# Kernel optimization log

Measured on AMD Instinct MI355X. Metric: run time of the kernel, lower is better.

## Reference

```python
import jax, jax.numpy as jnp
import numpy as np

N_TX, N_USER = 100000, 50000
F_TX, F_USER = 128, 64
HID, H, OUT = 64, 4, 32
E = 500000
SLOPE = 0.2  # PyG GATConv default negative_slope


def _gat(x_src, x_dst, src, dst, W, a_src, a_dst, bias, heads, ch, concat, n_dst):
    # PyG GATConv (shared lin for src/dst, add_self_loops=False)
    hs = (x_src @ W).reshape(-1, heads, ch)          # [Ns,H,C]
    hd = (x_dst @ W).reshape(-1, heads, ch)          # [Nd,H,C]
    als = jnp.einsum('nhc,hc->nh', hs, a_src)        # alpha_src per node
    ald = jnp.einsum('nhc,hc->nh', hd, a_dst)
    e = jax.nn.leaky_relu(als[src] + ald[dst], SLOPE)        # [E,H]
    emax = jax.ops.segment_max(e, dst, num_segments=n_dst)   # softmax per dst
    ex = jnp.exp(e - emax[dst])
    den = jax.ops.segment_sum(ex, dst, num_segments=n_dst)
    alpha = ex / (den[dst] + 1e-16)
    out = jax.ops.segment_sum(hs[src] * alpha[:, :, None], dst, num_segments=n_dst)
    out = out.reshape(n_dst, heads * ch) if concat else out.mean(axis=1)
    return out + bias


def setup_inputs() -> dict:
    key = jax.random.key(0)
    ks = iter(jax.random.split(key, 40))
    def nrm(shape, s=0.05):
        return jax.random.normal(next(ks), shape, dtype=jnp.float32) * s
    inp = {}
    inp['x_tx'] = jax.random.normal(next(ks), (N_TX, F_TX), dtype=jnp.float32)
    inp['x_user'] = jax.random.normal(next(ks), (N_USER, F_USER), dtype=jnp.float32)
    src_u = jax.random.randint(next(ks), (E,), 0, N_USER)
    dst_t = jax.random.randint(next(ks), (E,), 0, N_TX)
    inp['ei_u2t'] = jnp.stack([src_u, dst_t]).astype(jnp.int32)
    src_t = jax.random.randint(next(ks), (E,), 0, N_TX)
    dst_u = jax.random.randint(next(ks), (E,), 0, N_USER)
    inp['ei_t2u'] = jnp.stack([src_t, dst_u]).astype(jnp.int32)
    inp['Wp_tx'] = nrm((F_TX, HID)); inp['bp_tx'] = jnp.zeros((HID,), jnp.float32)
    inp['Wp_user'] = nrm((F_USER, HID)); inp['bp_user'] = jnp.zeros((HID,), jnp.float32)
    for et in ('u2t', 't2u'):
        inp[f'W1_{et}'] = nrm((HID, H * HID))
        inp[f'as1_{et}'] = nrm((H, HID)); inp[f'ad1_{et}'] = nrm((H, HID))
        inp[f'b1_{et}'] = jnp.zeros((H * HID,), jnp.float32)
        inp[f'W2_{et}'] = nrm((H * HID, OUT))
        inp[f'as2_{et}'] = nrm((1, OUT)); inp[f'ad2_{et}'] = nrm((1, OUT))
        inp[f'b2_{et}'] = jnp.zeros((OUT,), jnp.float32)
    inp['Wc'] = nrm((OUT, 1)); inp['bc'] = jnp.zeros((1,), jnp.float32)
    return inp


def reference(x_tx, x_user, ei_u2t, ei_t2u, Wp_tx, bp_tx, Wp_user, bp_user,
              W1_u2t, as1_u2t, ad1_u2t, b1_u2t, W1_t2u, as1_t2u, ad1_t2u, b1_t2u,
              W2_u2t, as2_u2t, ad2_u2t, b2_u2t, W2_t2u, as2_t2u, ad2_t2u, b2_t2u,
              Wc, bc):
    elu = jax.nn.elu
    h_tx = elu(x_tx @ Wp_tx + bp_tx)
    h_us = elu(x_user @ Wp_user + bp_user)
    # conv1: heads=H, concat=True (HeteroConv sum -> each dst has one edge type)
    t1 = _gat(h_us, h_tx, ei_u2t[0], ei_u2t[1], W1_u2t, as1_u2t, ad1_u2t, b1_u2t, H, HID, True, N_TX)
    u1 = _gat(h_tx, h_us, ei_t2u[0], ei_t2u[1], W1_t2u, as1_t2u, ad1_t2u, b1_t2u, H, HID, True, N_USER)
    t1, u1 = elu(t1), elu(u1)
    # conv2: heads=1, concat=False; only 'transaction' output feeds classifier
    t2 = elu(_gat(u1, t1, ei_u2t[0], ei_u2t[1], W2_u2t, as2_u2t, ad2_u2t, b2_u2t, 1, OUT, False, N_TX))
    return (t2 @ Wc + bc)[:, 0]
```

## Files before the change

### kernel.cpp

```cpp
#include <hip/hip_runtime.h>
#include <hip/hip_bf16.h>
#include <math.h>

#define N_TX   100000
#define N_USER 50000
#define F_TX   128
#define F_USER 64
#define HID    64
#define NH     4
#define OUTC   32
#define NE     500000
#define HC1    256
#define SLOPE  0.2f
#define NB_T   391
#define NB_U   196

__device__ __forceinline__ float elu_f(float x) { return x > 0.f ? x : (expf(x) - 1.f); }
__device__ __forceinline__ float lrelu_exp_fast(float x) { x = x > 0.f ? x : SLOPE * x; return __expf(x); }

__global__ __launch_bounds__(256) void gemm_kernel(const float* __restrict__ A,
    const float* __restrict__ B, const float* __restrict__ bias,
    float* __restrict__ C, int N, int K, int M, int act)
{
    __shared__ float As[16][65];
    __shared__ float Bs[16][65];
    const int tid = threadIdx.x;
    const int tx = tid % 16, ty = tid / 16;
    const int row0 = blockIdx.y * 64, col0 = blockIdx.x * 64;
    float acc[4][4] = {};
    for (int k0 = 0; k0 < K; k0 += 16) {
        #pragma unroll
        for (int i = 0; i < 4; ++i) {
            int idx = tid * 4 + i;
            int r = idx >> 4, kk = idx & 15;
            int gr = row0 + r;
            As[kk][r] = (gr < N) ? A[(size_t)gr * K + (k0 + kk)] : 0.f;
        }
        #pragma unroll
        for (int i = 0; i < 4; ++i) {
            int idx = tid * 4 + i;
            int kk = idx >> 6, c = idx & 63;
            int gc = col0 + c;
            Bs[kk][c] = (gc < M) ? B[(size_t)(k0 + kk) * M + gc] : 0.f;
        }
        __syncthreads();
        #pragma unroll
        for (int kk = 0; kk < 16; ++kk) {
            float a4[4], b4[4];
            #pragma unroll
            for (int i = 0; i < 4; ++i) a4[i] = As[kk][ty * 4 + i];
            #pragma unroll
            for (int j = 0; j < 4; ++j) b4[j] = Bs[kk][tx * 4 + j];
            #pragma unroll
            for (int i = 0; i < 4; ++i)
                #pragma unroll
                for (int j = 0; j < 4; ++j) acc[i][j] += a4[i] * b4[j];
        }
        __syncthreads();
    }
    #pragma unroll
    for (int i = 0; i < 4; ++i) {
        int r = row0 + ty * 4 + i;
        if (r >= N) continue;
        #pragma unroll
        for (int j = 0; j < 4; ++j) {
            int c = col0 + tx * 4 + j;
            if (c >= M) continue;
            float v = acc[i][j] + (bias ? bias[c] : 0.f);
            if (act == 1) v = elu_f(v);
            C[(size_t)r * M + c] = v;
        }
    }
}

__global__ __launch_bounds__(256) void gemm_proj_attn(const float* __restrict__ A,
    const float* __restrict__ B, const float* __restrict__ bias,
    float* __restrict__ C, int N, int K,
    const float* __restrict__ Ma, float* __restrict__ oa,
    const float* __restrict__ Mb, float* __restrict__ ob)
{
    __shared__ float As[16][65];
    __shared__ float Bs[16][65];
    const int tid = threadIdx.x;
    const int tx = tid % 16, ty = tid / 16;
    const int row0 = blockIdx.y * 64;
    float acc[4][4] = {};
    for (int k0 = 0; k0 < K; k0 += 16) {
        #pragma unroll
        for (int i = 0; i < 4; ++i) {
            int idx = tid * 4 + i;
            int r = idx >> 4, kk = idx & 15;
            int gr = row0 + r;
            As[kk][r] = (gr < N) ? A[(size_t)gr * K + (k0 + kk)] : 0.f;
        }
        #pragma unroll
        for (int i = 0; i < 4; ++i) {
            int idx = tid * 4 + i;
            int kk = idx >> 6, c = idx & 63;
            Bs[kk][c] = B[(size_t)(k0 + kk) * 64 + c];
        }
        __syncthreads();
        #pragma unroll
        for (int kk = 0; kk < 16; ++kk) {
            float a4[4], b4[4];
            #pragma unroll
            for (int i = 0; i < 4; ++i) a4[i] = As[kk][ty * 4 + i];
            #pragma unroll
            for (int j = 0; j < 4; ++j) b4[j] = Bs[kk][tx * 4 + j];
            #pragma unroll
            for (int i = 0; i < 4; ++i)
                #pragma unroll
                for (int j = 0; j < 4; ++j) acc[i][j] += a4[i] * b4[j];
        }
        __syncthreads();
    }
    const float4 ma0 = *(const float4*)(Ma + (tx * 4 + 0) * 4);
    const float4 ma1 = *(const float4*)(Ma + (tx * 4 + 1) * 4);
    const float4 ma2 = *(const float4*)(Ma + (tx * 4 + 2) * 4);
    const float4 ma3 = *(const float4*)(Ma + (tx * 4 + 3) * 4);
    const float4 mb0 = *(const float4*)(Mb + (tx * 4 + 0) * 4);
    const float4 mb1 = *(const float4*)(Mb + (tx * 4 + 1) * 4);
    const float4 mb2 = *(const float4*)(Mb + (tx * 4 + 2) * 4);
    const float4 mb3 = *(const float4*)(Mb + (tx * 4 + 3) * 4);
    const float4 bb  = *(const float4*)(bias + tx * 4);
    #pragma unroll
    for (int i = 0; i < 4; ++i) {
        int r = row0 + ty * 4 + i;
        bool wr = (r < N);
        float v0 = acc[i][0] + bb.x; v0 = v0 > 0.f ? v0 : (expf(v0) - 1.f);
        float v1 = acc[i][1] + bb.y; v1 = v1 > 0.f ? v1 : (expf(v1) - 1.f);
        float v2 = acc[i][2] + bb.z; v2 = v2 > 0.f ? v2 : (expf(v2) - 1.f);
        float v3 = acc[i][3] + bb.w; v3 = v3 > 0.f ? v3 : (expf(v3) - 1.f);
        if (wr) *(float4*)(C + (size_t)r * 64 + tx * 4) = make_float4(v0, v1, v2, v3);
        float pax = v0 * ma0.x + v1 * ma1.x + v2 * ma2.x + v3 * ma3.x;
        float pay = v0 * ma0.y + v1 * ma1.y + v2 * ma2.y + v3 * ma3.y;
        float paz = v0 * ma0.z + v1 * ma1.z + v2 * ma2.z + v3 * ma3.z;
        float paw = v0 * ma0.w + v1 * ma1.w + v2 * ma2.w + v3 * ma3.w;
        float pbx = v0 * mb0.x + v1 * mb1.x + v2 * mb2.x + v3 * mb3.x;
        float pby = v0 * mb0.y + v1 * mb1.y + v2 * mb2.y + v3 * mb3.y;
        float pbz = v0 * mb0.z + v1 * mb1.z + v2 * mb2.z + v3 * mb3.z;
        float pbw = v0 * mb0.w + v1 * mb1.w + v2 * mb2.w + v3 * mb3.w;
        #pragma unroll
        for (int off = 1; off < 16; off <<= 1) {
            pax += __shfl_xor(pax, off); pay += __shfl_xor(pay, off);
            paz += __shfl_xor(paz, off); paw += __shfl_xor(paw, off);
            pbx += __shfl_xor(pbx, off); pby += __shfl_xor(pby, off);
            pbz += __shfl_xor(pbz, off); pbw += __shfl_xor(pbw, off);
        }
        if (tx == 0 && wr) {
            *(float4*)(oa + (size_t)r * 4) = make_float4(pax, pay, paz, paw);
            *(float4*)(ob + (size_t)r * 4) = make_float4(pbx, pby, pbz, pbw);
        }
    }
}

struct AVArgs  { const float* W; const float* a; float* out; int K; int H; int C; };
struct AVArgs6 { AVArgs t[6]; };

__global__ void attn_vecs_kernel(AVArgs6 args)
{
    AVArgs A = args.t[blockIdx.x];
    int tid = threadIdx.x;
    if (tid < A.K * A.H) {
        int k = tid % A.K, h = tid / A.K;
        float s = 0.f;
        const float* wrow = A.W + (size_t)k * (A.H * A.C) + h * A.C;
        const float* arow = A.a + h * A.C;
        for (int c = 0; c < A.C; ++c) s += wrow[c] * arow[c];
        A.out[k * A.H + h] = s;
    }
}

__global__ __launch_bounds__(256) void hist2_kernel(const int* __restrict__ dst_t,
    const int* __restrict__ dst_u, int* __restrict__ deg_t, int* __restrict__ deg_u)
{
    int e = blockIdx.x * 256 + threadIdx.x;
    if (e < NE) atomicAdd(&deg_t[dst_t[e]], 1);
    else {
        e -= NE;
        if (e < NE) atomicAdd(&deg_u[dst_u[e]], 1);
    }
}

__global__ __launch_bounds__(256) void block_sum2_kernel(const int* __restrict__ deg_t,
    int* __restrict__ bsum_t, const int* __restrict__ deg_u, int* __restrict__ bsum_u)
{
    __shared__ int lds[256];
    int b = blockIdx.x, t = threadIdx.x;
    const int* deg; int* bsum; int Nd, lb;
    if (b < NB_T) { deg = deg_t; bsum = bsum_t; Nd = N_TX; lb = b; }
    else         { deg = deg_u; bsum = bsum_u; Nd = N_USER; lb = b - NB_T; }
    int i = lb * 256 + t;
    lds[t] = (i < Nd) ? deg[i] : 0;
    __syncthreads();
    for (int o = 128; o > 0; o >>= 1) {
        if (t < o) lds[t] += lds[t + o];
        __syncthreads();
    }
    if (t == 0) bsum[lb] = lds[0];
}

__global__ __launch_bounds__(512) void scan_bsum2_kernel(int* __restrict__ bt,
    int* __restrict__ bu)
{
    __shared__ int lds[512];
    int t = threadIdx.x;
    {
        int v = (t < NB_T) ? bt[t] : 0;
        lds[t] = v;
        __syncthreads();
        for (int o = 1; o < 512; o <<= 1) {
            int x = (t >= o) ? lds[t - o] : 0;
            __syncthreads();
            lds[t] += x;
            __syncthreads();
        }
        if (t < NB_T) bt[t] = lds[t] - v;
        __syncthreads();
    }
    {
        int v = (t < NB_U) ? bu[t] : 0;
        lds[t] = v;
        __syncthreads();
        for (int o = 1; o < 512; o <<= 1) {
            int x = (t >= o) ? lds[t - o] : 0;
            __syncthreads();
            lds[t] += x;
            __syncthreads();
        }
        if (t < NB_U) bu[t] = lds[t] - v;
    }
}

__global__ __launch_bounds__(256) void scan_final2_kernel(
    const int* __restrict__ deg_t, const int* __restrict__ be_t,
    int* __restrict__ rowptr_t, int* __restrict__ cur_t,
    const int* __restrict__ deg_u, const int* __restrict__ be_u,
    int* __restrict__ rowptr_u, int* __restrict__ cur_u)
{
    __shared__ int lds[256];
    int b = blockIdx.x, t = threadIdx.x;
    const int* deg; const int* be; int* rowptr; int* cursor; int Nd, lb;
    if (b < NB_T) { deg = deg_t; be = be_t; rowptr = rowptr_t; cursor = cur_t; Nd = N_TX; lb = b; }
    else         { deg = deg_u; be = be_u; rowptr = rowptr_u; cursor = cur_u; Nd = N_USER; lb = b - NB_T; }
    int i = lb * 256 + t;
    int v = (i < Nd) ? deg[i] : 0;
    lds[t] = v;
    __syncthreads();
    for (int o = 1; o < 256; o <<= 1) {
        int x = (t >= o) ? lds[t - o] : 0;
        __syncthreads();
        lds[t] += x;
        __syncthreads();
    }
    int excl = lds[t] - v + be[lb];
    if (i < Nd) {
        rowptr[i] = excl;
        cursor[i] = excl;
        if (i == Nd - 1) rowptr[Nd] = NE;
    }
}

__global__ __launch_bounds__(256) void scatter2_ew_kernel(
    const int* __restrict__ src_t, const int* __restrict__ dst_t,
    int* __restrict__ cur_t, int* __restrict__ csr_t, float* __restrict__ ew_t,
    const float* __restrict__ als_t, const float* __restrict__ ald_t,
    const int* __restrict__ src_u, const int* __restrict__ dst_u,
    int* __restrict__ cur_u, int* __restrict__ csr_u, float* __restrict__ ew_u,
    const float* __restrict__ als_u, const float* __restrict__ ald_u)
{
    int e = blockIdx.x * 256 + threadIdx.x;
    const int* srcA; const int* dstA; int* cur; int* csr; float* ew;
    const float* als; const float* ald;
    if (e < NE) {
        srcA = src_t; dstA = dst_t; cur = cur_t; csr = csr_t; ew = ew_t;
        als = als_t; ald = ald_t;
    } else {
        e -= NE;
        if (e >= NE) return;
        srcA = src_u; dstA = dst_u; cur = cur_u; csr = csr_u; ew = ew_u;
        als = als_u; ald = ald_u;
    }
    int s = srcA[e], d = dstA[e];
    int p = atomicAdd(&cur[d], 1);
    csr[p] = s;
    float4 a = *(const float4*)(als + (size_t)s * 4);
    float4 b = *(const float4*)(ald + (size_t)d * 4);
    float4 w;
    w.x = lrelu_exp_fast(a.x + b.x);
    w.y = lrelu_exp_fast(a.y + b.y);
    w.z = lrelu_exp_fast(a.z + b.z);
    w.w = lrelu_exp_fast(a.w + b.w);
    *(float4*)(ew + (size_t)p * 4) = w;
}

__device__ __forceinline__ void acc_edge(int s, int i, int lane,
    const float* __restrict__ ew, const float* __restrict__ hsrc,
    float& a0, float& a1, float& a2, float& a3,
    float& w0, float& w1, float& w2, float& w3)
{
    float4 e = *(const float4*)(ew + (size_t)i * 4);
    float x = hsrc[(size_t)s * 64 + lane];
    a0 = fmaf(e.x, x, a0); w0 += e.x;
    a1 = fmaf(e.y, x, a1); w1 += e.y;
    a2 = fmaf(e.z, x, a2); w2 += e.z;
    a3 = fmaf(e.w, x, a3); w3 += e.w;
}

__global__ __launch_bounds__(256) void agg_conv1_kernel(const int* __restrict__ rowptr,
    const int* __restrict__ csr, const float* __restrict__ hsrc,
    const float* __restrict__ ew, float* __restrict__ agg, int Nd)
{
    int d = blockIdx.x * 4 + (threadIdx.x >> 6);
    int lane = threadIdx.x & 63;
    if (d >= Nd) return;
    int beg = rowptr[d], end = rowptr[d + 1];
    float a0 = 0.f, a1 = 0.f, a2 = 0.f, a3 = 0.f;
    float w0 = 0.f, w1 = 0.f, w2 = 0.f, w3 = 0.f;
    int i = beg;
    for (; i + 2 <= end; i += 2) {
        int s0 = csr[i], s1 = csr[i + 1];
        acc_edge(s0, i,     lane, ew, hsrc, a0, a1, a2, a3, w0, w1, w2, w3);
        acc_edge(s1, i + 1, lane, ew, hsrc, a0, a1, a2, a3, w0, w1, w2, w3);
    }
    if (i < end)
        acc_edge(csr[i], i, lane, ew, hsrc, a0, a1, a2, a3, w0, w1, w2, w3);
    float* o = agg + (size_t)d * 256;
    o[lane]       = a0 / (w0 + 1e-16f);
    o[64 + lane]  = a1 / (w1 + 1e-16f);
    o[128 + lane] = a2 / (w2 + 1e-16f);
    o[192 + lane] = a3 / (w3 + 1e-16f);
}

#define ACC_STEP(i, XS, WV) \
    acc[i][0] = fmaf((XS), (WV).x, acc[i][0]); \
    acc[i][1] = fmaf((XS), (WV).y, acc[i][1]); \
    acc[i][2] = fmaf((XS), (WV).z, acc[i][2]); \
    acc[i][3] = fmaf((XS), (WV).w, acc[i][3]);
#define ACC4(i, XV) \
    ACC_STEP(i, (XV).x, w0) ACC_STEP(i, (XV).y, w1) \
    ACC_STEP(i, (XV).z, w2) ACC_STEP(i, (XV).w, w3)

__global__ __launch_bounds__(256) void transform_v6(
    const float* __restrict__ agg, const float* __restrict__ W1,
    const float* __restrict__ b1, const float* __restrict__ vvec,
    float* __restrict__ dot_part, float* __restrict__ rows_out,
    int Nd, int writeRows)
{
    constexpr int SXP = 68;
    __shared__ float sX[64 * SXP];
    __shared__ float sW[64 * 64];
    const int tid  = threadIdx.x;
    const int w    = tid >> 6;
    const int lane = tid & 63;
    const int h    = blockIdx.y;
    const int base = blockIdx.x * 64;

    #pragma unroll
    for (int it = 0; it < 4; ++it) {
        int r  = w * 16 + it * 4 + (lane >> 4);
        int c0 = (lane & 15) * 4;
        int g  = base + r;
        float4 v = make_float4(0.f, 0.f, 0.f, 0.f);
        if (g < Nd) v = *(const float4*)(agg + (size_t)g * 256 + h * 64 + c0);
        *(float4*)(sX + r * SXP + c0) = v;
    }
    #pragma unroll
    for (int it = 0; it < 4; ++it) {
        int c    = w * 16 + it * 4 + (lane >> 4);
        int col0 = (lane & 15) * 4;
        *(float4*)(sW + c * 64 + col0) =
            *(const float4*)(W1 + (size_t)c * 256 + h * 64 + col0);
    }
    __syncthreads();

    const int tx = tid & 15;
    const int ty = tid >> 4;
    float acc[4][4] = {};

    #pragma unroll 1
    for (int c0 = 0; c0 < 64; c0 += 4) {
        const float4 x0 = *(const float4*)(sX + (ty * 4 + 0) * SXP + c0);
        const float4 x1 = *(const float4*)(sX + (ty * 4 + 1) * SXP + c0);
        const float4 x2 = *(const float4*)(sX + (ty * 4 + 2) * SXP + c0);
        const float4 x3 = *(const float4*)(sX + (ty * 4 + 3) * SXP + c0);
        const float4 w0 = *(const float4*)(sW + (c0 + 0) * 64 + tx * 4);
        const float4 w1 = *(const float4*)(sW + (c0 + 1) * 64 + tx * 4);
        const float4 w2 = *(const float4*)(sW + (c0 + 2) * 64 + tx * 4);
        const float4 w3 = *(const float4*)(sW + (c0 + 3) * 64 + tx * 4);
        ACC4(0, x0)
        ACC4(1, x1)
        ACC4(2, x2)
        ACC4(3, x3)
    }

    const float4 bb = *(const float4*)(b1   + h * 64 + tx * 4);
    const float4 vv = *(const float4*)(vvec + h * 64 + tx * 4);
    float* dp = dot_part + (size_t)h * Nd;
    #pragma unroll
    for (int i = 0; i < 4; ++i) {
        int g = base + ty * 4 + i;
        if (g >= Nd) continue;
        float v0 = acc[i][0] + bb.x; v0 = v0 > 0.f ? v0 : (expf(v0) - 1.f);
        float v1 = acc[i][1] + bb.y; v1 = v1 > 0.f ? v1 : (expf(v1) - 1.f);
        float v2 = acc[i][2] + bb.z; v2 = v2 > 0.f ? v2 : (expf(v2) - 1.f);
        float v3 = acc[i][3] + bb.w; v3 = v3 > 0.f ? v3 : (expf(v3) - 1.f);
        if (writeRows)
            *(float4*)(rows_out + (size_t)g * 256 + h * 64 + tx * 4) =
                make_float4(v0, v1, v2, v3);
        float s = v0 * vv.x + v1 * vv.y + v2 * vv.z + v3 * vv.w;
        s += __shfl_xor(s, 1); s += __shfl_xor(s, 2);
        s += __shfl_xor(s, 4); s += __shfl_xor(s, 8);
        if (tx == 0) dp[g] = s;
    }
}

__global__ __launch_bounds__(256) void combine_parts(
    const float* __restrict__ ap, float* __restrict__ o1, int N1,
    const float* __restrict__ bp, float* __restrict__ o2, int N2)
{
    int i = blockIdx.x * 256 + threadIdx.x;
    if (i < N1) {
        o1[i] = ap[i] + ap[N1 + i] + ap[2 * N1 + i] + ap[3 * N1 + i];
    } else {
        int j = i - N1;
        if (j < N2)
            o2[j] = bp[j] + bp[N2 + j] + bp[2 * N2 + j] + bp[3 * N2 + j];
    }
}

__global__ __launch_bounds__(256) void conv2_fused_kernel(const int* __restrict__ rowptr,
    const int* __restrict__ csr, const float* __restrict__ hs2,
    const float* __restrict__ als2, const float* __restrict__ ald2,
    const float* __restrict__ b2, const float* __restrict__ Wc, const float* __restrict__ bc,
    float* __restrict__ out, int Nd)
{
    int d = blockIdx.x * 4 + (threadIdx.x >> 6);
    int lane = threadIdx.x & 63;
    if (d >= Nd) return;
    int beg = rowptr[d], end = rowptr[d + 1];
    float aldd = ald2[d];
    int half = lane >> 5, c = lane & 31;
    float acc = 0.f, wsum = 0.f;
    for (int i = beg + half; i < end; i += 2) {
        int s = csr[i];
        float w = lrelu_exp_fast(als2[s] + aldd);
        acc = fmaf(w, hs2[(size_t)s * 32 + c], acc);
        wsum += w;
    }
    acc  += __shfl_down(acc, 32);
    wsum += __shfl_down(wsum, 32);
    float val = 0.f;
    if (lane < 32) {
        float t2 = acc / (wsum + 1e-16f) + b2[c];
        t2 = t2 > 0.f ? t2 : (expf(t2) - 1.f);
        val = t2 * Wc[c];
    }
    #pragma unroll
    for (int o = 16; o > 0; o >>= 1) val += __shfl_down(val, o);
    if (lane == 0) out[d] = val + bc[0];
}

extern "C" void kernel_launch(void* const* d_in, const int* in_sizes, int n_in,
                              void* d_out, int out_size, void* d_ws, size_t ws_size,
                              hipStream_t stream)
{
    const float* x_tx    = (const float*)d_in[0];
    const float* x_user  = (const float*)d_in[1];
    const int*   ei_u2t  = (const int*)d_in[2];
    const int*   ei_t2u  = (const int*)d_in[3];
    const float* Wp_tx   = (const float*)d_in[4];
    const float* bp_tx   = (const float*)d_in[5];
    const float* Wp_user = (const float*)d_in[6];
    const float* bp_user = (const float*)d_in[7];
    const float* W1_u2t  = (const float*)d_in[8];
    const float* as1_u2t = (const float*)d_in[9];
    const float* ad1_u2t = (const float*)d_in[10];
    const float* b1_u2t  = (const float*)d_in[11];
    const float* W2_u2t  = (const float*)d_in[12];
    const float* as2_u2t = (const float*)d_in[13];
    const float* ad2_u2t = (const float*)d_in[14];
    const float* b2_u2t  = (const float*)d_in[15];
    const float* W1_t2u  = (const float*)d_in[16];
    const float* as1_t2u = (const float*)d_in[17];
    const float* ad1_t2u = (const float*)d_in[18];
    const float* b1_t2u  = (const float*)d_in[19];
    const float* Wc      = (const float*)d_in[24];
    const float* bc      = (const float*)d_in[25];
    float* out = (float*)d_out;
    float* ws  = (float*)d_ws;

    const int* src_u2t = ei_u2t;
    const int* dst_u2t = ei_u2t + NE;
    const int* src_t2u = ei_t2u;
    const int* dst_u   = ei_t2u + NE;

    float* h_tx   = ws;
    float* h_us   = ws + 6400000;
    float* hs2    = ws + 9600000;
    float* als2   = ws + 11200000;
    float* ald2   = ws + 11250000;
    float* als_us = ws + 11350000;
    float* ald_us = ws + 11550000;
    float* als_tx = ws + 11750000;
    float* ald_tx = ws + 12150000;
    float* agg    = ws + 12550000;
    float* avec   = ws + 38150000;
    float* ald2p = hs2;
    float* als2p = hs2 + 400000;
    float* ew_t   = ws + 38152000;
    float* ew_u   = ws + 40152000;
    int* ibase    = (int*)(ws + 42152000);
    int* deg_t    = ibase;
    int* deg_u    = ibase + 100000;
    int* rowptr_t = ibase + 150000;
    int* cur_t    = ibase + 250001;
    int* csr_t    = ibase + 350001;
    int* rowptr_u = ibase + 850001;
    int* cur_u    = ibase + 900002;
    int* csr_u    = ibase + 950002;
    int* bsum_t   = ibase + 1450002;
    int* bsum_u   = ibase + 1450514;

    float* Msrc_u2t = avec + 0;
    float* Mdst_u2t = avec + 256;
    float* Msrc_t2u = avec + 512;
    float* Mdst_t2u = avec + 768;
    float* vsrc2    = avec + 1024;
    float* vdst2    = avec + 1280;

    AVArgs6 av;
    av.t[0] = { W1_u2t, as1_u2t, Msrc_u2t, HID, NH, HID };
    av.t[1] = { W1_u2t, ad1_u2t, Mdst_u2t, HID, NH, HID };
    av.t[2] = { W1_t2u, as1_t2u, Msrc_t2u, HID, NH, HID };
    av.t[3] = { W1_t2u, ad1_t2u, Mdst_t2u, HID, NH, HID };
    av.t[4] = { W2_u2t, as2_u2t, vsrc2, HC1, 1, OUTC };
    av.t[5] = { W2_u2t, ad2_u2t, vdst2, HC1, 1, OUTC };
    attn_vecs_kernel<<<6, 256, 0, stream>>>(av);

    hipMemsetAsync(deg_t, 0, 150000 * sizeof(int), stream);

    hist2_kernel<<<(2 * NE + 255) / 256, 256, 0, stream>>>(dst_u2t, dst_u, deg_t, deg_u);
    block_sum2_kernel<<<NB_T + NB_U, 256, 0, stream>>>(deg_t, bsum_t, deg_u, bsum_u);
    scan_bsum2_kernel<<<1, 512, 0, stream>>>(bsum_t, bsum_u);
    scan_final2_kernel<<<NB_T + NB_U, 256, 0, stream>>>(
        deg_t, bsum_t, rowptr_t, cur_t, deg_u, bsum_u, rowptr_u, cur_u);

    gemm_proj_attn<<<dim3(1, (N_TX + 63) / 64), 256, 0, stream>>>(
        x_tx, Wp_tx, bp_tx, h_tx, N_TX, F_TX,
        Mdst_u2t, ald_tx, Msrc_t2u, als_tx);
    gemm_proj_attn<<<dim3(1, (N_USER + 63) / 64), 256, 0, stream>>>(
        x_user, Wp_user, bp_user, h_us, N_USER, F_USER,
        Msrc_u2t, als_us, Mdst_t2u, ald_us);

    scatter2_ew_kernel<<<(2 * NE + 255) / 256, 256, 0, stream>>>(
        src_u2t, dst_u2t, cur_t, csr_t, ew_t, als_us, ald_tx,
        src_t2u, dst_u,   cur_u, csr_u, ew_u, als_tx, ald_us);

    agg_conv1_kernel<<<(N_TX + 3) / 4, 256, 0, stream>>>(
        rowptr_t, csr_t, h_us, ew_t, agg, N_TX);
    transform_v6<<<dim3((N_TX + 63) / 64, NH), 256, 0, stream>>>(
        agg, W1_u2t, b1_u2t, vdst2, ald2p, nullptr, N_TX, 0);

    agg_conv1_kernel<<<(N_USER + 3) / 4, 256, 0, stream>>>(
        rowptr_u, csr_u, h_tx, ew_u, agg, N_USER);
    transform_v6<<<dim3((N_USER + 63) / 64, NH), 256, 0, stream>>>(
        agg, W1_t2u, b1_t2u, vsrc2, als2p, agg, N_USER, 1);
    float* u1 = agg;

    combine_parts<<<(N_TX + N_USER + 255) / 256, 256, 0, stream>>>(
        ald2p, ald2, N_TX, als2p, als2, N_USER);

    gemm_kernel<<<dim3(1, (N_USER + 63) / 64), 256, 0, stream>>>(
        u1, W2_u2t, nullptr, hs2, N_USER, HC1, OUTC, 0);
    conv2_fused_kernel<<<(N_TX + 3) / 4, 256, 0, stream>>>(
        rowptr_t, csr_t, hs2, als2, ald2, b2_u2t, Wc, bc, out, N_TX);
}
```

Before: 632.8 us.

## Keep W1 columns in registers and process all heads per block in transform

Rewrites the per-head conv1 output transform. Each thread now holds one 64-element column of W1 in registers, and each wave handles one head. A block stages 32 full 256-wide rows into LDS and reads them as wave-wide broadcasts. This removes the separate W tile staging and the 2D head grid, so each agg row is loaded once for all heads. In exchange it uses more registers, needs a 64-lane shuffle reduction per row, and does more LDS reads per FMA than the earlier 4x4 register tiling.

```diff
diff --git a/kernel.cpp b/kernel.cpp
--- a/kernel.cpp
+++ b/kernel.cpp
@@ -332,86 +332,59 @@
     o[192 + lane] = a3 / (w3 + 1e-16f);
 }
 
-#define ACC_STEP(i, XS, WV) \
-    acc[i][0] = fmaf((XS), (WV).x, acc[i][0]); \
-    acc[i][1] = fmaf((XS), (WV).y, acc[i][1]); \
-    acc[i][2] = fmaf((XS), (WV).z, acc[i][2]); \
-    acc[i][3] = fmaf((XS), (WV).w, acc[i][3]);
-#define ACC4(i, XV) \
-    ACC_STEP(i, (XV).x, w0) ACC_STEP(i, (XV).y, w1) \
-    ACC_STEP(i, (XV).z, w2) ACC_STEP(i, (XV).w, w3)
-
-__global__ __launch_bounds__(256) void transform_v6(
+#define TV7_GN 32
+
+#define LDW(q) const float4 Wr##q = make_float4( \
+    Wc0[(4*(q)+0)*256], Wc0[(4*(q)+1)*256], Wc0[(4*(q)+2)*256], Wc0[(4*(q)+3)*256]);
+
+#define DOT4(q) { const float4 xv = *(const float4*)(xrow + 4*(q)); \
+    acc = fmaf(xv.x, Wr##q.x, acc); acc = fmaf(xv.y, Wr##q.y, acc); \
+    acc = fmaf(xv.z, Wr##q.z, acc); acc = fmaf(xv.w, Wr##q.w, acc); }
+
+__global__ __launch_bounds__(256) void transform_v7(
     const float* __restrict__ agg, const float* __restrict__ W1,
     const float* __restrict__ b1, const float* __restrict__ vvec,
     float* __restrict__ dot_part, float* __restrict__ rows_out,
     int Nd, int writeRows)
 {
-    constexpr int SXP = 68;
-    __shared__ float sX[64 * SXP];
-    __shared__ float sW[64 * 64];
+    __shared__ float sX[TV7_GN * 256];
     const int tid  = threadIdx.x;
-    const int w    = tid >> 6;
+    const int h    = tid >> 6;
     const int lane = tid & 63;
-    const int h    = blockIdx.y;
-    const int base = blockIdx.x * 64;
+    const int base = blockIdx.x * TV7_GN;
+
+    const float* Wc0 = W1 + h * 64 + lane;
+    LDW(0)  LDW(1)  LDW(2)  LDW(3)  LDW(4)  LDW(5)  LDW(6)  LDW(7)
+    LDW(8)  LDW(9)  LDW(10) LDW(11) LDW(12) LDW(13) LDW(14) LDW(15)
+    const float breg = b1[h * 64 + lane];
+    const float vreg = vvec[h * 64 + lane];
 
     #pragma unroll
-    for (int it = 0; it < 4; ++it) {
-        int r  = w * 16 + it * 4 + (lane >> 4);
-        int c0 = (lane & 15) * 4;
-        int g  = base + r;
+    for (int it = 0; it < TV7_GN / 4; ++it) {
+        int r = h * (TV7_GN / 4) + it;
+        int g = base + r;
         float4 v = make_float4(0.f, 0.f, 0.f, 0.f);
-        if (g < Nd) v = *(const float4*)(agg + (size_t)g * 256 + h * 64 + c0);
-        *(float4*)(sX + r * SXP + c0) = v;
-    }
-    #pragma unroll
-    for (int it = 0; it < 4; ++it) {
-        int c    = w * 16 + it * 4 + (lane >> 4);
-        int col0 = (lane & 15) * 4;
-        *(float4*)(sW + c * 64 + col0) =
-            *(const float4*)(W1 + (size_t)c * 256 + h * 64 + col0);
+        if (g < Nd) v = *(const float4*)(agg + (size_t)g * 256 + lane * 4);
+        *(float4*)(sX + r * 256 + lane * 4) = v;
     }
     __syncthreads();
 
-    const int tx = tid & 15;
-    const int ty = tid >> 4;
-    float acc[4][4] = {};
+    float* dp = dot_part + (size_t)h * Nd;
 
     #pragma unroll 1
-    for (int c0 = 0; c0 < 64; c0 += 4) {
-        const float4 x0 = *(const float4*)(sX + (ty * 4 + 0) * SXP + c0);
-        const float4 x1 = *(const float4*)(sX + (ty * 4 + 1) * SXP + c0);
-        const float4 x2 = *(const float4*)(sX + (ty * 4 + 2) * SXP + c0);
-        const float4 x3 = *(const float4*)(sX + (ty * 4 + 3) * SXP + c0);
-        const float4 w0 = *(const float4*)(sW + (c0 + 0) * 64 + tx * 4);
-        const float4 w1 = *(const float4*)(sW + (c0 + 1) * 64 + tx * 4);
-        const float4 w2 = *(const float4*)(sW + (c0 + 2) * 64 + tx * 4);
-        const float4 w3 = *(const float4*)(sW + (c0 + 3) * 64 + tx * 4);
-        ACC4(0, x0)
-        ACC4(1, x1)
-        ACC4(2, x2)
-        ACC4(3, x3)
-    }
-
-    const float4 bb = *(const float4*)(b1   + h * 64 + tx * 4);
-    const float4 vv = *(const float4*)(vvec + h * 64 + tx * 4);
-    float* dp = dot_part + (size_t)h * Nd;
-    #pragma unroll
-    for (int i = 0; i < 4; ++i) {
-        int g = base + ty * 4 + i;
-        if (g >= Nd) continue;
-        float v0 = acc[i][0] + bb.x; v0 = v0 > 0.f ? v0 : (expf(v0) - 1.f);
-        float v1 = acc[i][1] + bb.y; v1 = v1 > 0.f ? v1 : (expf(v1) - 1.f);
-        float v2 = acc[i][2] + bb.z; v2 = v2 > 0.f ? v2 : (expf(v2) - 1.f);
-        float v3 = acc[i][3] + bb.w; v3 = v3 > 0.f ? v3 : (expf(v3) - 1.f);
-        if (writeRows)
-            *(float4*)(rows_out + (size_t)g * 256 + h * 64 + tx * 4) =
-                make_float4(v0, v1, v2, v3);
-        float s = v0 * vv.x + v1 * vv.y + v2 * vv.z + v3 * vv.w;
-        s += __shfl_xor(s, 1); s += __shfl_xor(s, 2);
-        s += __shfl_xor(s, 4); s += __shfl_xor(s, 8);
-        if (tx == 0) dp[g] = s;
+    for (int n = 0; n < TV7_GN; ++n) {
+        const float* xrow = sX + n * 256 + h * 64;
+        float acc = breg;
+        DOT4(0)  DOT4(1)  DOT4(2)  DOT4(3)  DOT4(4)  DOT4(5)  DOT4(6)  DOT4(7)
+        DOT4(8)  DOT4(9)  DOT4(10) DOT4(11) DOT4(12) DOT4(13) DOT4(14) DOT4(15)
+        float v = acc > 0.f ? acc : (expf(acc) - 1.f);
+        int g = base + n;
+        if (writeRows && g < Nd)
+            rows_out[(size_t)g * 256 + h * 64 + lane] = v;
+        float s = v * vreg;
+        s += __shfl_xor(s, 1);  s += __shfl_xor(s, 2);  s += __shfl_xor(s, 4);
+        s += __shfl_xor(s, 8);  s += __shfl_xor(s, 16); s += __shfl_xor(s, 32);
+        if (lane == 0 && g < Nd) dp[g] = s;
     }
 }
 
@@ -559,12 +532,12 @@
 
     agg_conv1_kernel<<<(N_TX + 3) / 4, 256, 0, stream>>>(
         rowptr_t, csr_t, h_us, ew_t, agg, N_TX);
-    transform_v6<<<dim3((N_TX + 63) / 64, NH), 256, 0, stream>>>(
+    transform_v7<<<(N_TX + TV7_GN - 1) / TV7_GN, 256, 0, stream>>>(
         agg, W1_u2t, b1_u2t, vdst2, ald2p, nullptr, N_TX, 0);
 
     agg_conv1_kernel<<<(N_USER + 3) / 4, 256, 0, stream>>>(
         rowptr_u, csr_u, h_tx, ew_u, agg, N_USER);
-    transform_v6<<<dim3((N_USER + 63) / 64, NH), 256, 0, stream>>>(
+    transform_v7<<<(N_USER + TV7_GN - 1) / TV7_GN, 256, 0, stream>>>(
         agg, W1_t2u, b1_t2u, vsrc2, als2p, agg, N_USER, 1);
     float* u1 = agg;
 
```

After: 675.6 us. +6.8%, slower.
